# Kernel optimization log

Measured on AMD Instinct MI355X. Metric: run time of the kernel, lower is better.

## Reference

```python
import jax, jax.numpy as jnp
import numpy as np

D_MODEL = 1024
N_HEADS = 16
N_GROUPS = 4
D_K = D_MODEL // N_HEADS
HEADS_PER_GROUP = N_HEADS // N_GROUPS


def rope(x):
    # x: [b, s, d]; rotate using half-split concat (NOT interleaved), matching source
    s, d = x.shape[1], x.shape[2]
    theta = 1.0 / (10000.0 ** (jnp.arange(d // 2, dtype=jnp.float32) / (d // 2)))
    ang = jnp.arange(s, dtype=jnp.float32)[:, None] * theta[None, :]  # [s, d/2]
    cos, sin = jnp.cos(ang), jnp.sin(ang)
    xe, xo = x[..., 0::2], x[..., 1::2]
    return jnp.concatenate([xe * cos - xo * sin, xe * sin + xo * cos], axis=-1)


def setup_inputs() -> dict:
    key = jax.random.key(0)
    k1, k2, k3, k4, k5 = jax.random.split(key, 5)
    b, s = 1, 2048
    scale = 0.02
    X = jax.random.normal(k1, (b, s, D_MODEL), dtype=jnp.float32)
    W_q = jax.random.normal(k2, (D_MODEL, D_MODEL), dtype=jnp.float32) * scale
    W_k = jax.random.normal(k3, (N_GROUPS * D_K, D_MODEL), dtype=jnp.float32) * scale
    W_v = jax.random.normal(k4, (N_GROUPS * D_K, D_MODEL), dtype=jnp.float32) * scale
    W_o = jax.random.normal(k5, (D_MODEL, D_MODEL), dtype=jnp.float32) * scale
    return {"X": X, "W_q": W_q, "W_k": W_k, "W_v": W_v, "W_o": W_o}


def reference(X, W_q, W_k, W_v, W_o):
    b, s, _ = X.shape
    Xr = rope(X)
    Q = (Xr @ W_q.T).reshape(b, s, N_HEADS, D_K).transpose(0, 2, 1, 3)
    K = (Xr @ W_k.T).reshape(b, s, N_GROUPS, D_K).transpose(0, 2, 1, 3)
    V = (Xr @ W_v.T).reshape(b, s, N_GROUPS, D_K).transpose(0, 2, 1, 3)
    Q = Q.reshape(b, N_GROUPS, HEADS_PER_GROUP, s, D_K)
    scores = jnp.einsum('bghsd,bgtd->bghst', Q, K) / jnp.sqrt(jnp.float32(D_K))
    mask = jnp.triu(jnp.ones((s, s), dtype=scores.dtype), k=1) * (-1e9)
    attn = jax.nn.softmax(scores + mask, axis=-1)
    out = jnp.einsum('bghst,bgtd->bghsd', attn, V)  # [b,g,h,s,dk]
    out = out.reshape(b, N_HEADS, s, D_K).transpose(0, 2, 1, 3).reshape(b, s, D_MODEL)
    return out @ W_o.T
```

## Files before the change

### kernel.cpp

```cpp
#include <hip/hip_runtime.h>
#include <hip/hip_bf16.h>

#define S_LEN   2048
#define D_MODEL 1024
#define N_HEADS 16
#define N_GROUPS 4
#define D_K     64
#define KV_DIM  (N_GROUPS * D_K)

typedef __hip_bfloat16 bf16;
typedef unsigned short u16;
typedef __attribute__((ext_vector_type(8))) short bfrag;
typedef __attribute__((ext_vector_type(4))) float ffrag;
typedef __attribute__((ext_vector_type(4))) unsigned int u32x4;

__device__ __forceinline__ float b2f(u16 u) {
    return __uint_as_float(((unsigned)u) << 16);
}
__device__ __forceinline__ u16 f2bu(float f) {
    bf16 h = __float2bfloat16(f);
    return __builtin_bit_cast(u16, h);
}
__device__ __forceinline__ unsigned cvt_pk_bf16(float lo, float hi) {
    unsigned r;
    asm("v_cvt_pk_bf16_f32 %0, %1, %2" : "=v"(r) : "v"(lo), "v"(hi));
    return r;
}
__device__ __forceinline__ float ex2(float x) {
#if __has_builtin(__builtin_amdgcn_exp2f)
    return __builtin_amdgcn_exp2f(x);
#else
    return __expf(x * 0.69314718f);
#endif
}

typedef __attribute__((address_space(3))) u16 lds_u16;
typedef __attribute__((address_space(1))) const u16 glb_u16;
__device__ __forceinline__ void gld_lds16(const u16* g, u16* l) {
    __builtin_amdgcn_global_load_lds((glb_u16*)g, (lds_u16*)l, 16, 0, 0);
}

__device__ __forceinline__ int probe_f32(const u16* p) {
    int lane = threadIdx.x & 63;
    int e0 = (p[lane] >> 7) & 0xFF;
    int e1 = (p[lane + 64] >> 7) & 0xFF;
    int c = ((e0 < 100 || e0 > 140) ? 1 : 0) + ((e1 < 100 || e1 > 140) ? 1 : 0);
    unsigned long long b1 = __ballot(c >= 1);
    unsigned long long b2 = __ballot(c >= 2);
    return ((__popcll(b1) + __popcll(b2)) > 16) ? 1 : 0;
}

__global__ void probe5_kernel(const u16* __restrict__ p0, const u16* __restrict__ p1,
                              const u16* __restrict__ p2, const u16* __restrict__ p3,
                              const u16* __restrict__ p4, int* __restrict__ mode) {
    if (blockIdx.x != 0) return;
    const u16* ps[5] = {p0, p1, p2, p3, p4};
    int lane = threadIdx.x & 63;
    for (int t = 0; t < 5; t++) {
        int e0 = (ps[t][lane] >> 7) & 0xFF;
        int e1 = (ps[t][lane + 64] >> 7) & 0xFF;
        int c = ((e0 < 100 || e0 > 140) ? 1 : 0) + ((e1 < 100 || e1 > 140) ? 1 : 0);
        unsigned long long b1 = __ballot(c >= 1);
        unsigned long long b2 = __ballot(c >= 2);
        if (lane == 0) mode[t] = ((__popcll(b1) + __popcll(b2)) > 16) ? 1 : 0;
    }
}

__global__ __launch_bounds__(512)
void prep_kernel(const void* __restrict__ Xin, u16* __restrict__ Xr,
                 const void* __restrict__ Wq, const void* __restrict__ Wk,
                 const void* __restrict__ Wv, const void* __restrict__ Wo,
                 u16* __restrict__ WB, u16* __restrict__ WoB) {
    int b = blockIdx.x;
    if (b < S_LEN) {
        int md = probe_f32((const u16*)Xin);
        int i = b;
        int j = threadIdx.x;
        float freq = ex2(-(float)j * 0.025952563241307518f);
        float ang  = (float)i * freq;
        float sv, cv;
        sincosf(ang, &sv, &cv);
        int base = i * D_MODEL;
        float xe, xo;
        if (md) {
            float2 xv = *(const float2*)&((const float*)Xin)[base + 2 * j];
            xe = xv.x; xo = xv.y;
        } else {
            ushort2 xv = *(const ushort2*)&((const u16*)Xin)[base + 2 * j];
            xe = b2f(xv.x); xo = b2f(xv.y);
        }
        Xr[base + j]       = f2bu(xe * cv - xo * sv);
        Xr[base + 512 + j] = f2bu(xe * sv + xo * cv);
    } else {
        int bid = b - S_LEN;
        const void* src; u16* dst; int goff;
        if (bid < 256)      { src = Wq; dst = WB;               goff = bid; }
        else if (bid < 320) { src = Wk; dst = WB + 1024 * 1024; goff = bid - 256; }
        else if (bid < 384) { src = Wv; dst = WB + 1280 * 1024; goff = bid - 320; }
        else                { src = Wo; dst = WoB;              goff = bid - 384; }
        int md = probe_f32((const u16*)src);
        size_t g = (size_t)goff * 512 + threadIdx.x;
        if (md) {
            const float* f = (const float*)src + g * 8;
            float4 v0 = *(const float4*)f;
            float4 v1 = *(const float4*)(f + 4);
            u16 t[8] = {f2bu(v0.x), f2bu(v0.y), f2bu(v0.z), f2bu(v0.w),
                        f2bu(v1.x), f2bu(v1.y), f2bu(v1.z), f2bu(v1.w)};
            *(uint4*)(dst + g * 8) = *(const uint4*)t;
        } else {
            *(uint4*)(dst + g * 8) = *(const uint4*)((const u16*)src + g * 8);
        }
    }
}

__global__ __launch_bounds__(512)
void rope_kernel(const void* __restrict__ Xin, u16* __restrict__ Xr) {
    int md = probe_f32((const u16*)Xin);
    int i = blockIdx.x;
    int j = threadIdx.x;
    float freq = ex2(-(float)j * 0.025952563241307518f);
    float ang  = (float)i * freq;
    float sv, cv;
    sincosf(ang, &sv, &cv);
    int base = i * D_MODEL;
    float xe, xo;
    if (md) {
        float2 xv = *(const float2*)&((const float*)Xin)[base + 2 * j];
        xe = xv.x; xo = xv.y;
    } else {
        ushort2 xv = *(const ushort2*)&((const u16*)Xin)[base + 2 * j];
        xe = b2f(xv.x); xo = b2f(xv.y);
    }
    Xr[base + j]       = f2bu(xe * cv - xo * sv);
    Xr[base + 512 + j] = f2bu(xe * sv + xo * cv);
}

template<int MODE>
__global__ __launch_bounds__(256)
void gemm_fast(const u16* __restrict__ A, const u16* __restrict__ WBm,
               u16* __restrict__ Qm, u16* __restrict__ Km, u16* __restrict__ Vm,
               float* __restrict__ Cf) {
    __shared__ u16 As[2][8192];
    __shared__ u16 Bs[2][4096];
    const int tid = threadIdx.x;
    const int w = tid >> 6, lane = tid & 63, quad = lane >> 4, lcol = lane & 15;
    const int m0 = blockIdx.y * 128;
    const int n0 = blockIdx.x * 64;

    const int arl   = lane >> 3;
    const int colsw = ((lane & 7) ^ arl) * 8;

    const u16* ap[4]; const u16* bp[2];
    #pragma unroll
    for (int c = 0; c < 4; c++)
        ap[c] = A + (size_t)(m0 + (c * 4 + w) * 8 + arl) * 1024 + colsw;
    #pragma unroll
    for (int c = 0; c < 2; c++)
        bp[c] = WBm + (size_t)(n0 + (c * 4 + w) * 8 + arl) * 1024 + colsw;

    const int abase = (w * 32 + lcol) * 64;
    const int koff0 = (quad * 8) ^ ((lcol & 7) * 8);
    const int koff1 = koff0 ^ 32;

    ffrag acc[2][4];
    #pragma unroll
    for (int rf = 0; rf < 2; rf++)
        #pragma unroll
        for (int ct = 0; ct < 4; ct++) acc[rf][ct] = (ffrag)0.0f;

    #pragma unroll
    for (int c = 0; c < 4; c++) gld_lds16(ap[c], &As[0][(c * 4 + w) * 512]);
    #pragma unroll
    for (int c = 0; c < 2; c++) gld_lds16(bp[c], &Bs[0][(c * 4 + w) * 512]);
    __syncthreads();

    int cur = 0;
    for (int k0 = 0; k0 < D_MODEL; k0 += 64) {
        if (k0 + 64 < D_MODEL) {
            const int nb = cur ^ 1;
            #pragma unroll
            for (int c = 0; c < 4; c++)
                gld_lds16(ap[c] + k0 + 64, &As[nb][(c * 4 + w) * 512]);
            #pragma unroll
            for (int c = 0; c < 2; c++)
                gld_lds16(bp[c] + k0 + 64, &Bs[nb][(c * 4 + w) * 512]);
        }

        const u16* Ab = &As[cur][0];
        const u16* Bb = &Bs[cur][0];
        const bfrag a00 = *(const bfrag*)&Ab[abase + koff0];
        const bfrag a10 = *(const bfrag*)&Ab[abase + 1024 + koff0];
        const bfrag a01 = *(const bfrag*)&Ab[abase + koff1];
        const bfrag a11 = *(const bfrag*)&Ab[abase + 1024 + koff1];
        #pragma unroll
        for (int ct = 0; ct < 4; ct++) {
            const int bb = (ct * 16 + lcol) * 64;
            const bfrag b0 = *(const bfrag*)&Bb[bb + koff0];
            acc[0][ct] = __builtin_amdgcn_mfma_f32_16x16x32_bf16(a00, b0, acc[0][ct], 0, 0, 0);
            acc[1][ct] = __builtin_amdgcn_mfma_f32_16x16x32_bf16(a10, b0, acc[1][ct], 0, 0, 0);
            const bfrag b1 = *(const bfrag*)&Bb[bb + koff1];
            acc[0][ct] = __builtin_amdgcn_mfma_f32_16x16x32_bf16(a01, b1, acc[0][ct], 0, 0, 0);
            acc[1][ct] = __builtin_amdgcn_mfma_f32_16x16x32_bf16(a11, b1, acc[1][ct], 0, 0, 0);
        }
        __syncthreads();
        cur ^= 1;
    }

    if (MODE == 0) {
        if (n0 < 1280) {
            u16* Cp; int ldc, nc;
            if (n0 < 1024) { Cp = Qm; ldc = 1024; nc = n0; }
            else           { Cp = Km; ldc = 256;  nc = n0 - 1024; }
            #pragma unroll
            for (int rf = 0; rf < 2; rf++)
                #pragma unroll
                for (int ct = 0; ct < 4; ct++)
                    #pragma unroll
                    for (int r = 0; r < 4; r++) {
                        int row = m0 + w * 32 + rf * 16 + quad * 4 + r;
                        Cp[(size_t)row * ldc + nc + ct * 16 + lcol] = f2bu(acc[rf][ct][r]);
                    }
        } else {
            const int nc = n0 - 1280;
            #pragma unroll
            for (int rf = 0; rf < 2; rf++)
                #pragma unroll
                for (int ct = 0; ct < 4; ct++)
                    #pragma unroll
                    for (int r = 0; r < 4; r++) {
                        int row = m0 + w * 32 + rf * 16 + quad * 4 + r;
                        int col = nc + ct * 16 + lcol;
                        Vm[(size_t)col * S_LEN + row] = f2bu(acc[rf][ct][r]);
                    }
        }
    } else {
        #pragma unroll
        for (int rf = 0; rf < 2; rf++)
            #pragma unroll
            for (int ct = 0; ct < 4; ct++)
                #pragma unroll
                for (int r = 0; r < 4; r++) {
                    int row = m0 + w * 32 + rf * 16 + quad * 4 + r;
                    Cf[(size_t)row * D_MODEL + n0 + ct * 16 + lcol] = acc[rf][ct][r];
                }
    }
}

__device__ __forceinline__ void stageB(u16* dst, const void* Bv, size_t off, int md) {
    if (md) {
        const float* Bf = (const float*)Bv;
        float4 b0 = *(const float4*)&Bf[off];
        float4 b1 = *(const float4*)&Bf[off + 4];
        u16 t[8] = {f2bu(b0.x), f2bu(b0.y), f2bu(b0.z), f2bu(b0.w),
                    f2bu(b1.x), f2bu(b1.y), f2bu(b1.z), f2bu(b1.w)};
        *(uint4*)dst = *(const uint4*)t;
    } else {
        *(uint4*)dst = *(const uint4*)&((const u16*)Bv)[off];
    }
}

__global__ __launch_bounds__(256)
void qkv_mfma(const u16* __restrict__ Xr, const void* __restrict__ Wq,
              const void* __restrict__ Wk, const void* __restrict__ Wv,
              u16* __restrict__ Qm, u16* __restrict__ Km, u16* __restrict__ Vm,
              const int* __restrict__ mode) {
    __shared__ u16 As[128][36];
    __shared__ u16 Bs[64][36];
    const int tid = threadIdx.x;
    const int w = tid >> 6, lane = tid & 63, quad = lane >> 4, lcol = lane & 15;
    const int m0 = blockIdx.y * 128;
    const int n0 = blockIdx.x * 64;

    const void* Bv; int nb, md;
    if (n0 < 1024)       { Bv = Wq; nb = n0;        md = mode[1]; }
    else if (n0 < 1280)  { Bv = Wk; nb = n0 - 1024; md = mode[2]; }
    else                 { Bv = Wv; nb = n0 - 1280; md = mode[3]; }

    ffrag acc[2][4];
    #pragma unroll
    for (int rf = 0; rf < 2; rf++)
        #pragma unroll
        for (int ct = 0; ct < 4; ct++) acc[rf][ct] = (ffrag)0.0f;

    const int arow = tid >> 2, akc = tid & 3;
    for (int k0 = 0; k0 < D_MODEL; k0 += 32) {
        *(uint4*)&As[arow][akc * 8] =
            *(const uint4*)&Xr[(size_t)(m0 + arow) * D_MODEL + k0 + akc * 8];
        *(uint4*)&As[arow + 64][akc * 8] =
            *(const uint4*)&Xr[(size_t)(m0 + arow + 64) * D_MODEL + k0 + akc * 8];
        stageB(&Bs[arow][akc * 8], Bv, (size_t)(nb + arow) * D_MODEL + k0 + akc * 8, md);
        __syncthreads();
        const bfrag a0 = *(const bfrag*)&As[w * 32 + lcol][quad * 8];
        const bfrag a1 = *(const bfrag*)&As[w * 32 + 16 + lcol][quad * 8];
        #pragma unroll
        for (int ct = 0; ct < 4; ct++) {
            const bfrag b = *(const bfrag*)&Bs[ct * 16 + lcol][quad * 8];
            acc[0][ct] = __builtin_amdgcn_mfma_f32_16x16x32_bf16(a0, b, acc[0][ct], 0, 0, 0);
            acc[1][ct] = __builtin_amdgcn_mfma_f32_16x16x32_bf16(a1, b, acc[1][ct], 0, 0, 0);
        }
        __syncthreads();
    }

    if (n0 < 1280) {
        u16* Cp; int ldc, nc;
        if (n0 < 1024) { Cp = Qm; ldc = 1024; nc = n0; }
        else           { Cp = Km; ldc = 256;  nc = n0 - 1024; }
        #pragma unroll
        for (int rf = 0; rf < 2; rf++)
            #pragma unroll
            for (int ct = 0; ct < 4; ct++)
                #pragma unroll
                for (int r = 0; r < 4; r++) {
                    int row = m0 + w * 32 + rf * 16 + quad * 4 + r;
                    Cp[(size_t)row * ldc + nc + ct * 16 + lcol] = f2bu(acc[rf][ct][r]);
                }
    } else {
        const int nc = n0 - 1280;
        #pragma unroll
        for (int rf = 0; rf < 2; rf++)
            #pragma unroll
            for (int ct = 0; ct < 4; ct++)
                #pragma unroll
                for (int r = 0; r < 4; r++) {
                    int row = m0 + w * 32 + rf * 16 + quad * 4 + r;
                    int col = nc + ct * 16 + lcol;
                    Vm[(size_t)col * S_LEN + row] = f2bu(acc[rf][ct][r]);
                }
    }
}

__global__ __launch_bounds__(256)
void oproj_mfma(const u16* __restrict__ A, const void* __restrict__ B,
                float* __restrict__ C, const int* __restrict__ mode) {
    __shared__ u16 As[128][36];
    __shared__ u16 Bs[64][36];
    const int tid = threadIdx.x;
    const int w = tid >> 6, lane = tid & 63, quad = lane >> 4, lcol = lane & 15;
    const int m0 = blockIdx.y * 128;
    const int n0 = blockIdx.x * 64;
    const int md = mode[4];

    ffrag acc[2][4];
    #pragma unroll
    for (int rf = 0; rf < 2; rf++)
        #pragma unroll
        for (int ct = 0; ct < 4; ct++) acc[rf][ct] = (ffrag)0.0f;

    const int arow = tid >> 2, akc = tid & 3;
    for (int k0 = 0; k0 < D_MODEL; k0 += 32) {
        *(uint4*)&As[arow][akc * 8] =
            *(const uint4*)&A[(size_t)(m0 + arow) * D_MODEL + k0 + akc * 8];
        *(uint4*)&As[arow + 64][akc * 8] =
            *(const uint4*)&A[(size_t)(m0 + arow + 64) * D_MODEL + k0 + akc * 8];
        stageB(&Bs[arow][akc * 8], B, (size_t)(n0 + arow) * D_MODEL + k0 + akc * 8, md);
        __syncthreads();
        const bfrag a0 = *(const bfrag*)&As[w * 32 + lcol][quad * 8];
        const bfrag a1 = *(const bfrag*)&As[w * 32 + 16 + lcol][quad * 8];
        #pragma unroll
        for (int ct = 0; ct < 4; ct++) {
            const bfrag b = *(const bfrag*)&Bs[ct * 16 + lcol][quad * 8];
            acc[0][ct] = __builtin_amdgcn_mfma_f32_16x16x32_bf16(a0, b, acc[0][ct], 0, 0, 0);
            acc[1][ct] = __builtin_amdgcn_mfma_f32_16x16x32_bf16(a1, b, acc[1][ct], 0, 0, 0);
        }
        __syncthreads();
    }

    #pragma unroll
    for (int rf = 0; rf < 2; rf++)
        #pragma unroll
        for (int ct = 0; ct < 4; ct++)
            #pragma unroll
            for (int r = 0; r < 4; r++) {
                int row = m0 + w * 32 + rf * 16 + quad * 4 + r;
                C[(size_t)row * D_MODEL + n0 + ct * 16 + lcol] = acc[rf][ct][r];
            }
}

template<int CS, int SF>
__global__ __launch_bounds__(256)
void attn_part(const u16* __restrict__ Q, const u16* __restrict__ K,
               const u16* __restrict__ Vt, float* __restrict__ OpF,
               u16* __restrict__ OpH, float2* __restrict__ ml2) {
    const int bid = blockIdx.x;
    const int cidx = bid >> 4;
    const int h = bid & 15;
    const int g = h >> 2;

    int i, c;
    if (CS == 3) {
        if (cidx < 8)       { i = cidx;                  c = 0; }
        else if (cidx < 24) { i = 8 + ((cidx - 8) >> 1); c = (cidx - 8) & 1; }
        else if (cidx < 48) { int q = (cidx - 24) / 3;   i = 16 + q; c = (cidx - 24) - 3 * q; }
        else                { i = 24 + ((cidx - 48) >> 2); c = (cidx - 48) & 3; }
    } else {
        if (cidx < 16) { i = cidx; c = 0; }
        else           { i = 16 + ((cidx - 16) >> 1); c = (cidx - 16) & 1; }
    }
    const int i0 = i * 64;
    const int tile0 = c << CS;
    const int tlast = min(i, ((c + 1) << CS) - 1);
    const int nt = tlast - tile0 + 1;

    const int tid  = threadIdx.x;
    const int w    = tid >> 6;
    const int lane = tid & 63;
    const int quad = lane >> 4;
    const int lcol = lane & 15;

    __shared__ u16 Ks[2][64][72];
    __shared__ u16 Vts[2][64][72];

    const int qi = i0 + w * 16 + lcol;
    const bfrag qb0 = *(const bfrag*)&Q[(size_t)qi * D_MODEL + h * 64 + quad * 8];
    const bfrag qb1 = *(const bfrag*)&Q[(size_t)qi * D_MODEL + h * 64 + 32 + quad * 8];

    ffrag oacc[4];
    #pragma unroll
    for (int ct = 0; ct < 4; ct++) oacc[ct] = (ffrag)0.0f;
    float m_run = -1e30f, l_run = 0.0f;

    const int key0 = tid & 63, dc0 = tid >> 6;
    const int vd0 = tid >> 3, vch = tid & 7;
    const int vpos0 = 32 * (vch >> 2) + 16 * (vch & 1) + 4 * ((vch >> 1) & 1);
    const u16* vbase0 = &Vt[(size_t)(g * 64 + vd0) * S_LEN];
    const u16* vbase1 = &Vt[(size_t)(g * 64 + vd0 + 32) * S_LEN];

    int jp = tile0 * 64;
    uint4 kpre0 = *(const uint4*)&K[(size_t)(jp + key0) * KV_DIM + g * 64 + dc0 * 8];
    uint4 kpre1 = *(const uint4*)&K[(size_t)(jp + key0) * KV_DIM + g * 64 + (dc0 + 4) * 8];
    uint4 vpre0 = *(const uint4*)&vbase0[jp + vch * 8];
    uint4 vpre1 = *(const uint4*)&vbase1[jp + vch * 8];

    {
        *(uint4*)&Ks[0][key0][dc0 * 8]       = kpre0;
        *(uint4*)&Ks[0][key0][(dc0 + 4) * 8] = kpre1;
        *(uint2*)&Vts[0][vd0][vpos0]          = make_uint2(vpre0.x, vpre0.y);
        *(uint2*)&Vts[0][vd0][vpos0 + 8]      = make_uint2(vpre0.z, vpre0.w);
        *(uint2*)&Vts[0][vd0 + 32][vpos0]     = make_uint2(vpre1.x, vpre1.y);
        *(uint2*)&Vts[0][vd0 + 32][vpos0 + 8] = make_uint2(vpre1.z, vpre1.w);
    }

    const float CF = 0.18033688f;
    int cur = 0;

    for (int tt = 0; tt < nt; tt++) {
        const int j0 = (tile0 + tt) * 64;

        if (tt + 1 < nt) {
            const int j0n = (tile0 + tt + 1) * 64;
            kpre0 = *(const uint4*)&K[(size_t)(j0n + key0) * KV_DIM + g * 64 + dc0 * 8];
            kpre1 = *(const uint4*)&K[(size_t)(j0n + key0) * KV_DIM + g * 64 + (dc0 + 4) * 8];
            vpre0 = *(const uint4*)&vbase0[j0n + vch * 8];
            vpre1 = *(const uint4*)&vbase1[j0n + vch * 8];
        }
        __syncthreads();

        ffrag sacc[4];
        #pragma unroll
        for (int ct = 0; ct < 4; ct++) sacc[ct] = (ffrag)0.0f;
        __builtin_amdgcn_s_setprio(1);
        #pragma unroll
        for (int ct = 0; ct < 4; ct++) {
            const bfrag kb0 = *(const bfrag*)&Ks[cur][ct * 16 + lcol][quad * 8];
            sacc[ct] = __builtin_amdgcn_mfma_f32_16x16x32_bf16(kb0, qb0, sacc[ct], 0, 0, 0);
            const bfrag kb1 = *(const bfrag*)&Ks[cur][ct * 16 + lcol][32 + quad * 8];
            sacc[ct] = __builtin_amdgcn_mfma_f32_16x16x32_bf16(kb1, qb1, sacc[ct], 0, 0, 0);
        }
        __builtin_amdgcn_s_setprio(0);

        float sv[4][4];
        if (tile0 + tt == i) {
            #pragma unroll
            for (int ct = 0; ct < 4; ct++)
                #pragma unroll
                for (int r = 0; r < 4; r++) {
                    int kj = j0 + ct * 16 + quad * 4 + r;
                    sv[ct][r] = (kj <= qi) ? sacc[ct][r] : -1e30f;
                }
        } else {
            #pragma unroll
            for (int ct = 0; ct < 4; ct++)
                #pragma unroll
                for (int r = 0; r < 4; r++) sv[ct][r] = sacc[ct][r];
        }

        float mx = sv[0][0];
        #pragma unroll
        for (int ct = 0; ct < 4; ct++)
            #pragma unroll
            for (int r = 0; r < 4; r++) mx = fmaxf(mx, sv[ct][r]);
        mx = fmaxf(mx, __shfl_xor(mx, 16, 64));
        mx = fmaxf(mx, __shfl_xor(mx, 32, 64));

        if (!__all(mx <= m_run + 44.0f)) {
            float mnew = fmaxf(m_run, mx);
            float al = ex2((m_run - mnew) * CF);
            m_run = mnew;
            l_run *= al;
            #pragma unroll
            for (int r = 0; r < 4; r++) {
                float ar = __shfl(al, quad * 4 + r, 64);
                #pragma unroll
                for (int ct = 0; ct < 4; ct++) oacc[ct][r] *= ar;
            }
        }

        const float mc = m_run * CF;
        float rs = 0.0f;
        #pragma unroll
        for (int ct = 0; ct < 4; ct++)
            #pragma unroll
            for (int r = 0; r < 4; r++) {
                float p = ex2(sv[ct][r] * CF - mc);
                sv[ct][r] = p;
                rs += p;
            }
        rs += __shfl_xor(rs, 16, 64);
        rs += __shfl_xor(rs, 32, 64);
        l_run += rs;

        u32x4 pw0, pw1;
        pw0[0] = cvt_pk_bf16(sv[0][0], sv[0][1]);
        pw0[1] = cvt_pk_bf16(sv[0][2], sv[0][3]);
        pw0[2] = cvt_pk_bf16(sv[1][0], sv[1][1]);
        pw0[3] = cvt_pk_bf16(sv[1][2], sv[1][3]);
        pw1[0] = cvt_pk_bf16(sv[2][0], sv[2][1]);
        pw1[1] = cvt_pk_bf16(sv[2][2], sv[2][3]);
        pw1[2] = cvt_pk_bf16(sv[3][0], sv[3][1]);
        pw1[3] = cvt_pk_bf16(sv[3][2], sv[3][3]);
        const bfrag pa0 = __builtin_bit_cast(bfrag, pw0);
        const bfrag pa1 = __builtin_bit_cast(bfrag, pw1);

        __builtin_amdgcn_s_setprio(1);
        #pragma unroll
        for (int ct = 0; ct < 4; ct++) {
            const bfrag vb0 = *(const bfrag*)&Vts[cur][ct * 16 + lcol][quad * 8];
            oacc[ct] = __builtin_amdgcn_mfma_f32_16x16x32_bf16(pa0, vb0, oacc[ct], 0, 0, 0);
            const bfrag vb1 = *(const bfrag*)&Vts[cur][ct * 16 + lcol][32 + quad * 8];
            oacc[ct] = __builtin_amdgcn_mfma_f32_16x16x32_bf16(pa1, vb1, oacc[ct], 0, 0, 0);
        }
        __builtin_amdgcn_s_setprio(0);

        if (tt + 1 < nt) {
            const int nb = cur ^ 1;
            *(uint4*)&Ks[nb][key0][dc0 * 8]       = kpre0;
            *(uint4*)&Ks[nb][key0][(dc0 + 4) * 8] = kpre1;
            *(uint2*)&Vts[nb][vd0][vpos0]          = make_uint2(vpre0.x, vpre0.y);
            *(uint2*)&Vts[nb][vd0][vpos0 + 8]      = make_uint2(vpre0.z, vpre0.w);
            *(uint2*)&Vts[nb][vd0 + 32][vpos0]     = make_uint2(vpre1.x, vpre1.y);
            *(uint2*)&Vts[nb][vd0 + 32][vpos0 + 8] = make_uint2(vpre1.z, vpre1.w);
        }
        cur ^= 1;
    }

    #pragma unroll
    for (int ct = 0; ct < 4; ct++)
        #pragma unroll
        for (int r = 0; r < 4; r++) {
            int row = w * 16 + quad * 4 + r;
            size_t off = (size_t)bid * 4096 + row * 64 + ct * 16 + lcol;
            if (SF) OpF[off] = oacc[ct][r];
            else    OpH[off] = f2bu(oacc[ct][r]);
        }
    if (quad == 0)
        ml2[(size_t)bid * 64 + w * 16 + lcol] = make_float2(m_run * 0.125f, l_run);
}

template<int CS, int SF>
__global__ __launch_bounds__(256)
void attn_combine(const float* __restrict__ OpF, const u16* __restrict__ OpH,
                  const float2* __restrict__ ml2, u16* __restrict__ Om) {
    const int row = blockIdx.x;
    const int i = row >> 6;
    const int r = row & 63;
    const int t = threadIdx.x;
    const int h = t >> 4;
    const int d = (t & 15) * 4;
    const int nc = (i >> CS) + 1;
    int pfx;
    if (CS == 3)
        pfx = (i < 8) ? i : (i < 16) ? 8 + 2 * (i - 8)
            : (i < 24) ? 24 + 3 * (i - 16) : 48 + 4 * (i - 24);
    else
        pfx = (i < 16) ? i : 16 + 2 * (i - 16);

    float M = -1e30f;
    for (int c = 0; c < nc; c++) {
        float2 m = ml2[(size_t)((pfx + c) * 16 + h) * 64 + r];
        M = fmaxf(M, m.x);
    }
    float L = 0.0f;
    float acc[4] = {0.0f, 0.0f, 0.0f, 0.0f};
    for (int c = 0; c < nc; c++) {
        float2 m = ml2[(size_t)((pfx + c) * 16 + h) * 64 + r];
        float wgt = __expf(m.x - M);
        L += m.y * wgt;
        size_t off = (size_t)((pfx + c) * 16 + h) * 4096 + r * 64 + d;
        if (SF) {
            float4 v = *(const float4*)&OpF[off];
            acc[0] += v.x * wgt; acc[1] += v.y * wgt;
            acc[2] += v.z * wgt; acc[3] += v.w * wgt;
        } else {
            ushort4 v = *(const ushort4*)&OpH[off];
            acc[0] += b2f(v.x) * wgt; acc[1] += b2f(v.y) * wgt;
            acc[2] += b2f(v.z) * wgt; acc[3] += b2f(v.w) * wgt;
        }
    }
    float inv = 1.0f / L;
    #pragma unroll
    for (int k = 0; k < 4; k++)
        Om[(size_t)row * D_MODEL + h * 64 + d + k] = f2bu(acc[k] * inv);
}

extern "C" void kernel_launch(void* const* d_in, const int* in_sizes, int n_in,
                              void* d_out, int out_size, void* d_ws, size_t ws_size,
                              hipStream_t stream) {
    const void* X  = d_in[0];
    const void* Wq = d_in[1];
    const void* Wk = d_in[2];
    const void* Wv = d_in[3];
    const void* Wo = d_in[4];
    float* out = (float*)d_out;

    u16* XrB = (u16*)d_out;

    int* mode = (int*)d_ws;
    u16* Qm = (u16*)((char*)d_ws + 64);
    u16* Km = Qm + (size_t)S_LEN * D_MODEL;
    u16* Vm = Km + (size_t)S_LEN * KV_DIM;
    u16* Om = Vm + (size_t)S_LEN * KV_DIM;

    const size_t needA    = 10485824ULL + 20971520ULL + 655360ULL;
    const size_t needFull = needA + 3145728ULL + 2097152ULL;

    if (ws_size >= needFull) {
        float*  OpF = (float*)((char*)d_ws + 10485824);
        float2* ml2 = (float2*)((char*)d_ws + 10485824 + 20971520);
        u16*    WB  = (u16*)((char*)d_ws + needA);
        u16*    WoB = WB + (size_t)1536 * 1024;

        prep_kernel<<<S_LEN + 640, 512, 0, stream>>>(X, XrB, Wq, Wk, Wv, Wo, WB, WoB);
        gemm_fast<0><<<dim3(24, 16), 256, 0, stream>>>(XrB, WB, Qm, Km, Vm, nullptr);
        attn_part<3, 1><<<80 * 16, 256, 0, stream>>>(Qm, Km, Vm, OpF, nullptr, ml2);
        attn_combine<3, 1><<<S_LEN, 256, 0, stream>>>(OpF, nullptr, ml2, Om);
        gemm_fast<1><<<dim3(16, 16), 256, 0, stream>>>(Om, WoB, nullptr, nullptr, nullptr, out);
    } else {
        rope_kernel<<<S_LEN, 512, 0, stream>>>(X, XrB);
        probe5_kernel<<<1, 64, 0, stream>>>(
            (const u16*)X, (const u16*)Wq, (const u16*)Wk, (const u16*)Wv,
            (const u16*)Wo, mode);
        qkv_mfma<<<dim3((D_MODEL + 2 * KV_DIM) / 64, S_LEN / 128), 256, 0, stream>>>(
            XrB, Wq, Wk, Wv, Qm, Km, Vm, mode);
        if (ws_size >= needA) {
            float*  OpF = (float*)((char*)d_ws + 10485824);
            float2* ml2 = (float2*)((char*)d_ws + 10485824 + 20971520);
            attn_part<3, 1><<<80 * 16, 256, 0, stream>>>(Qm, Km, Vm, OpF, nullptr, ml2);
            attn_combine<3, 1><<<S_LEN, 256, 0, stream>>>(OpF, nullptr, ml2, Om);
        } else {
            u16*    OpH = (u16*)d_out;
            float2* ml2 = (float2*)((char*)d_out + (size_t)768 * 4096 * 2);
            attn_part<4, 0><<<48 * 16, 256, 0, stream>>>(Qm, Km, Vm, nullptr, OpH, ml2);
            attn_combine<4, 0><<<S_LEN, 256, 0, stream>>>(nullptr, OpH, ml2, Om);
        }
        oproj_mfma<<<dim3(D_MODEL / 64, S_LEN / 128), 256, 0, stream>>>(Om, Wo, out, mode);
    }
}
```

Before: 141.8 us.

## Fuse split-KV combine into attention via last-block atomic counter

Measured after the change: 363.9 us. +156.7%, slower.

```diff
diff --git a/kernel.cpp b/kernel.cpp
--- a/kernel.cpp
+++ b/kernel.cpp
@@ -25,6 +25,11 @@
     unsigned r;
     asm("v_cvt_pk_bf16_f32 %0, %1, %2" : "=v"(r) : "v"(lo), "v"(hi));
     return r;
+}
+__device__ __forceinline__ float max3f(float a, float b, float c) {
+    float d;
+    asm("v_max3_f32 %0, %1, %2, %3" : "=v"(d) : "v"(a), "v"(b), "v"(c));
+    return d;
 }
 __device__ __forceinline__ float ex2(float x) {
 #if __has_builtin(__builtin_amdgcn_exp2f)
@@ -70,7 +75,8 @@
 void prep_kernel(const void* __restrict__ Xin, u16* __restrict__ Xr,
                  const void* __restrict__ Wq, const void* __restrict__ Wk,
                  const void* __restrict__ Wv, const void* __restrict__ Wo,
-                 u16* __restrict__ WB, u16* __restrict__ WoB) {
+                 u16* __restrict__ WB, u16* __restrict__ WoB,
+                 int* __restrict__ cnt) {
     int b = blockIdx.x;
     if (b < S_LEN) {
         int md = probe_f32((const u16*)Xin);
@@ -93,6 +99,7 @@
         Xr[base + 512 + j] = f2bu(xe * sv + xo * cv);
     } else {
         int bid = b - S_LEN;
+        if (bid == 0) cnt[threadIdx.x] = 0;
         const void* src; u16* dst; int goff;
         if (bid < 256)      { src = Wq; dst = WB;               goff = bid; }
         else if (bid < 320) { src = Wk; dst = WB + 1024 * 1024; goff = bid - 256; }
@@ -144,8 +151,12 @@
     __shared__ u16 Bs[2][4096];
     const int tid = threadIdx.x;
     const int w = tid >> 6, lane = tid & 63, quad = lane >> 4, lcol = lane & 15;
-    const int m0 = blockIdx.y * 128;
-    const int n0 = blockIdx.x * 64;
+
+    const int flat = blockIdx.y * gridDim.x + blockIdx.x;
+    const int cpx  = (gridDim.x * gridDim.y) >> 3;
+    const int ns   = (flat & 7) * cpx + (flat >> 3);
+    const int m0 = (ns / gridDim.x) * 128;
+    const int n0 = (ns % gridDim.x) * 64;
 
     const int arl   = lane >> 3;
     const int colsw = ((lane & 7) ^ arl) * 8;
@@ -376,11 +387,12 @@
             }
 }
 
-template<int CS, int SF>
+template<int CS, int SF, int CB>
 __global__ __launch_bounds__(256)
 void attn_part(const u16* __restrict__ Q, const u16* __restrict__ K,
                const u16* __restrict__ Vt, float* __restrict__ OpF,
-               u16* __restrict__ OpH, float2* __restrict__ ml2) {
+               u16* __restrict__ OpH, float2* __restrict__ ml2,
+               int* __restrict__ cnt, u16* __restrict__ Om) {
     const int bid = blockIdx.x;
     const int cidx = bid >> 4;
     const int h = bid & 15;
@@ -409,6 +421,7 @@
 
     __shared__ u16 Ks[2][64][72];
     __shared__ u16 Vts[2][64][72];
+    __shared__ int scnt;
 
     const int qi = i0 + w * 16 + lcol;
     const bfrag qb0 = *(const bfrag*)&Q[(size_t)qi * D_MODEL + h * 64 + quad * 8];
@@ -484,11 +497,12 @@
                 for (int r = 0; r < 4; r++) sv[ct][r] = sacc[ct][r];
         }
 
-        float mx = sv[0][0];
-        #pragma unroll
-        for (int ct = 0; ct < 4; ct++)
-            #pragma unroll
-            for (int r = 0; r < 4; r++) mx = fmaxf(mx, sv[ct][r]);
+        float t0 = max3f(sv[0][0], sv[0][1], sv[0][2]);
+        float t1 = max3f(sv[0][3], sv[1][0], sv[1][1]);
+        float t2 = max3f(sv[1][2], sv[1][3], sv[2][0]);
+        float t3 = max3f(sv[2][1], sv[2][2], sv[2][3]);
+        float t4 = max3f(sv[3][0], sv[3][1], sv[3][2]);
+        float mx = fmaxf(max3f(t0, t1, t2), max3f(t3, t4, sv[3][3]));
         mx = fmaxf(mx, __shfl_xor(mx, 16, 64));
         mx = fmaxf(mx, __shfl_xor(mx, 32, 64));
 
@@ -564,6 +578,46 @@
         }
     if (quad == 0)
         ml2[(size_t)bid * 64 + w * 16 + lcol] = make_float2(m_run * 0.125f, l_run);
+
+    if (CB) {
+        __threadfence();
+        if (tid == 0) scnt = atomicAdd(&cnt[i * 16 + h], 1);
+        __syncthreads();
+        if (scnt == (i >> CS)) {
+            __threadfence();
+            int pfx;
+            if (CS == 3)
+                pfx = (i < 8) ? i : (i < 16) ? 8 + 2 * (i - 8)
+                    : (i < 24) ? 24 + 3 * (i - 16) : 48 + 4 * (i - 24);
+            else
+                pfx = (i < 16) ? i : 16 + 2 * (i - 16);
+            const int nc = (i >> CS) + 1;
+            #pragma unroll
+            for (int it = 0; it < 4; it++) {
+                int idx = tid + it * 256;
+                int r = idx >> 4;
+                int d = (idx & 15) * 4;
+                float M = -1e30f;
+                for (int cc = 0; cc < nc; cc++)
+                    M = fmaxf(M, ml2[(size_t)((pfx + cc) * 16 + h) * 64 + r].x);
+                float L = 0.0f;
+                float a0 = 0, a1 = 0, a2 = 0, a3 = 0;
+                for (int cc = 0; cc < nc; cc++) {
+                    float2 m = ml2[(size_t)((pfx + cc) * 16 + h) * 64 + r];
+                    float wgt = __expf(m.x - M);
+                    L += m.y * wgt;
+                    float4 v = *(const float4*)
+                        &OpF[(size_t)((pfx + cc) * 16 + h) * 4096 + r * 64 + d];
+                    a0 += v.x * wgt; a1 += v.y * wgt; a2 += v.z * wgt; a3 += v.w * wgt;
+                }
+                float inv = 1.0f / L;
+                ushort4 o;
+                o.x = f2bu(a0 * inv); o.y = f2bu(a1 * inv);
+                o.z = f2bu(a2 * inv); o.w = f2bu(a3 * inv);
+                *(ushort4*)&Om[(size_t)(i * 64 + r) * D_MODEL + h * 64 + d] = o;
+            }
+        }
+    }
 }
 
 template<int CS, int SF>
@@ -631,18 +685,18 @@
     u16* Om = Vm + (size_t)S_LEN * KV_DIM;
 
     const size_t needA    = 10485824ULL + 20971520ULL + 655360ULL;
-    const size_t needFull = needA + 3145728ULL + 2097152ULL;
+    const size_t needFull = needA + 3145728ULL + 2097152ULL + 2048ULL;
 
     if (ws_size >= needFull) {
         float*  OpF = (float*)((char*)d_ws + 10485824);
         float2* ml2 = (float2*)((char*)d_ws + 10485824 + 20971520);
         u16*    WB  = (u16*)((char*)d_ws + needA);
         u16*    WoB = WB + (size_t)1536 * 1024;
-
-        prep_kernel<<<S_LEN + 640, 512, 0, stream>>>(X, XrB, Wq, Wk, Wv, Wo, WB, WoB);
+        int*    cnt = (int*)((char*)d_ws + needA + 3145728ULL + 2097152ULL);
+
+        prep_kernel<<<S_LEN + 640, 512, 0, stream>>>(X, XrB, Wq, Wk, Wv, Wo, WB, WoB, cnt);
         gemm_fast<0><<<dim3(24, 16), 256, 0, stream>>>(XrB, WB, Qm, Km, Vm, nullptr);
-        attn_part<3, 1><<<80 * 16, 256, 0, stream>>>(Qm, Km, Vm, OpF, nullptr, ml2);
-        attn_combine<3, 1><<<S_LEN, 256, 0, stream>>>(OpF, nullptr, ml2, Om);
+        attn_part<3, 1, 1><<<80 * 16, 256, 0, stream>>>(Qm, Km, Vm, OpF, nullptr, ml2, cnt, Om);
         gemm_fast<1><<<dim3(16, 16), 256, 0, stream>>>(Om, WoB, nullptr, nullptr, nullptr, out);
     } else {
         rope_kernel<<<S_LEN, 512, 0, stream>>>(X, XrB);
@@ -654,12 +708,14 @@
         if (ws_size >= needA) {
             float*  OpF = (float*)((char*)d_ws + 10485824);
             float2* ml2 = (float2*)((char*)d_ws + 10485824 + 20971520);
-            attn_part<3, 1><<<80 * 16, 256, 0, stream>>>(Qm, Km, Vm, OpF, nullptr, ml2);
+            attn_part<3, 1, 0><<<80 * 16, 256, 0, stream>>>(Qm, Km, Vm, OpF, nullptr, ml2,
+                                                            nullptr, nullptr);
             attn_combine<3, 1><<<S_LEN, 256, 0, stream>>>(OpF, nullptr, ml2, Om);
         } else {
             u16*    OpH = (u16*)d_out;
             float2* ml2 = (float2*)((char*)d_out + (size_t)768 * 4096 * 2);
-            attn_part<4, 0><<<48 * 16, 256, 0, stream>>>(Qm, Km, Vm, nullptr, OpH, ml2);
+            attn_part<4, 0, 0><<<48 * 16, 256, 0, stream>>>(Qm, Km, Vm, nullptr, OpH, ml2,
+                                                            nullptr, nullptr);
             attn_combine<4, 0><<<S_LEN, 256, 0, stream>>>(nullptr, OpH, ml2, Om);
         }
         oproj_mfma<<<dim3(D_MODEL / 64, S_LEN / 128), 256, 0, stream>>>(Om, Wo, out, mode);
```
